# Kernel optimization log

Hardware: AMD Instinct MI355X
Metric: run time of the kernel (lower is better)

## Reference

```python
import jax, jax.numpy as jnp
import numpy as np

K = 3          # pooling factor (init k)
H_OUT = 8      # number of bilinear heads
H_DIM = 512    # hidden dim after pooling
BN_EPS = 1e-5
NEG_INF = -jnp.inf


def setup_inputs() -> dict:
    key = jax.random.key(0)
    ks = jax.random.split(key, 8)
    b, vn, qn, vd, qd = 16, 256, 256, 512, 768
    hk = H_DIM * K
    return {
        "v": jax.random.normal(ks[0], (b, vn, vd), jnp.float32),
        "q": jax.random.normal(ks[1], (b, qn, qd), jnp.float32),
        "Wv": jax.random.normal(ks[2], (hk, vd), jnp.float32) * 0.05,
        "bv": jax.random.normal(ks[3], (hk,), jnp.float32) * 0.05,
        "Wq": jax.random.normal(ks[4], (hk, qd), jnp.float32) * 0.05,
        "bq": jax.random.normal(ks[5], (hk,), jnp.float32) * 0.05,
        "h_mat": jax.random.normal(ks[6], (1, H_OUT, 1, hk), jnp.float32),
        "h_bias": jax.random.normal(ks[7], (1, H_OUT, 1, 1), jnp.float32),
        "bn_gamma": jnp.ones((H_DIM,), jnp.float32),
        "bn_beta": jnp.zeros((H_DIM,), jnp.float32),
    }


def _forward(v, q, Wv, bv, Wq, bq, h_mat, h_bias, bn_gamma, bn_beta):
    # FCNet (eval mode: dropout is identity; weight_norm folded into W)
    v_ = jax.nn.relu(jnp.einsum("bvd,kd->bvk", v, Wv) + bv)   # [b, vn, h_dim*k]
    q_ = jax.nn.relu(jnp.einsum("bqd,kd->bqk", q, Wq) + bq)   # [b, qn, h_dim*k]

    # Bilinear attention maps: [b, h_out, vn, qn]
    att = jnp.einsum("xhyk,bvk,bqk->bhvq", h_mat, v_, q_) + h_bias

    # v_mask / q_mask (all-zero token rows masked to -inf)
    v_zero = jnp.sum(jnp.abs(v), axis=2) == 0                  # [b, vn]
    q_zero = jnp.sum(jnp.abs(q), axis=2) == 0                  # [b, qn]
    att = jnp.where(v_zero[:, None, :, None], NEG_INF, att)
    att = jnp.where(q_zero[:, None, None, :], NEG_INF, att)

    # Fused per-head attention pooling, summed over heads (original Python loop)
    fused = jnp.einsum("bhvq,bqk->bhvk", att, q_)
    logits_k = jnp.einsum("bvk,bhvk->bk", v_, fused)           # [b, h_dim*k]

    # AvgPool1d(k, stride=k) * k  == sum over groups of k
    b = logits_k.shape[0]
    logits = logits_k.reshape(b, H_DIM, K).sum(axis=2)         # [b, h_dim]

    # BatchNorm1d (training-mode batch statistics, biased variance)
    mu = logits.mean(axis=0)
    var = logits.var(axis=0)
    logits = (logits - mu) * jax.lax.rsqrt(var + BN_EPS) * bn_gamma + bn_beta
    return logits, att


def reference(v, q, Wv, bv, Wq, bq, h_mat, h_bias, bn_gamma, bn_beta):
    return _forward(v, q, Wv, bv, Wq, bq, h_mat, h_bias, bn_gamma, bn_beta)
```

## Files before the change

kernel.cpp:

```cpp
#include <hip/hip_runtime.h>
#include <math.h>

#define BB    16
#define VN    256
#define QN    256
#define VD    512
#define QD    768
#define HK    1536
#define HDIM  512

typedef _Float16 half8 __attribute__((ext_vector_type(8)));
typedef _Float16 half4 __attribute__((ext_vector_type(4)));
typedef float f32x4 __attribute__((ext_vector_type(4)));

__global__ __launch_bounds__(256) void conv_mask2(
    const float* __restrict__ v, const float* __restrict__ q,
    _Float16* __restrict__ v16, _Float16* __restrict__ q16,
    float* __restrict__ vz, float* __restrict__ qz) {
    int which = blockIdx.y;
    const float* src = which ? q : v;
    _Float16* dst = which ? q16 : v16;
    float* outz = which ? qz : vz;
    int D = which ? QD : VD;
    int w = threadIdx.x >> 6, ln = threadIdx.x & 63;
    int row = blockIdx.x * 4 + w;
    const float* p = src + (size_t)row * D;
    _Float16* d = dst + (size_t)row * D;
    float s = 0.f;
    for (int c = ln * 4; c < D; c += 256) {
        float4 x = *(const float4*)(p + c);
        s += fabsf(x.x) + fabsf(x.y) + fabsf(x.z) + fabsf(x.w);
        half4 hh = {(_Float16)x.x, (_Float16)x.y, (_Float16)x.z, (_Float16)x.w};
        *(half4*)(d + c) = hh;
    }
    for (int off = 32; off > 0; off >>= 1) s += __shfl_down(s, off);
    if (ln == 0) outz[row] = (s == 0.f) ? 1.f : 0.f;
}

__global__ __launch_bounds__(256) void conv_w3(
    const float* __restrict__ Wv, _Float16* __restrict__ Wv16, int n4v,
    const float* __restrict__ Wq, _Float16* __restrict__ Wq16, int n4q,
    const float* __restrict__ hm, _Float16* __restrict__ hs16) {
    if (blockIdx.y == 2) {
        int k = blockIdx.x * 256 + threadIdx.x;
        if (k >= HK) return;
        float s = 0.f;
#pragma unroll
        for (int h = 0; h < 8; ++h) {
            float x = hm[h * HK + k];
            s += x;
            hs16[h * HK + k] = (_Float16)x;
        }
        hs16[8 * HK + k] = (_Float16)s;
        return;
    }
    const float* src = blockIdx.y ? Wq : Wv;
    _Float16* dst = blockIdx.y ? Wq16 : Wv16;
    int n4 = blockIdx.y ? n4q : n4v;
    int i = blockIdx.x * 256 + threadIdx.x;
    if (i < n4) {
        float4 x = ((const float4*)src)[i];
        half4 h = {(_Float16)x.x, (_Float16)x.y, (_Float16)x.z, (_Float16)x.w};
        ((half4*)dst)[i] = h;
    }
}

__global__ __launch_bounds__(128) void proj_lds(
    const _Float16* __restrict__ Ain, const _Float16* __restrict__ W16,
    const float* __restrict__ bias, _Float16* __restrict__ C16, int K) {
    __shared__ _Float16 As[64 * 64];
    __shared__ _Float16 Bs[64 * 64];
    int m0 = blockIdx.y * 64, n0 = blockIdx.x * 64;
    int t = threadIdx.x;
    int w = t >> 6, ln = t & 63, quad = ln >> 4, r16 = ln & 15;
    int arow = t >> 3, aseg = t & 7;
    int sg = aseg ^ (arow & 7);
    const _Float16* ApG = Ain + (size_t)(m0 + arow) * K + aseg * 8;
    const _Float16* BpG = W16 + (size_t)(n0 + arow) * K + aseg * 8;
    half8 ra[4], rb[4];
#pragma unroll
    for (int c = 0; c < 4; ++c) {
        ra[c] = *(const half8*)(ApG + (size_t)c * 16 * K);
        rb[c] = *(const half8*)(BpG + (size_t)c * 16 * K);
    }
    f32x4 acc[2][4] = {};
    for (int k0 = 0; k0 < K; k0 += 64) {
        __syncthreads();
#pragma unroll
        for (int c = 0; c < 4; ++c) {
            *(half8*)&As[(c * 16 + arow) * 64 + sg * 8] = ra[c];
            *(half8*)&Bs[(c * 16 + arow) * 64 + sg * 8] = rb[c];
        }
        __syncthreads();
        if (k0 + 64 < K) {
#pragma unroll
            for (int c = 0; c < 4; ++c) {
                ra[c] = *(const half8*)(ApG + (size_t)c * 16 * K + k0 + 64);
                rb[c] = *(const half8*)(BpG + (size_t)c * 16 * K + k0 + 64);
            }
        }
#pragma unroll
        for (int kc = 0; kc < 2; ++kc) {
            half8 af[2], bf[4];
#pragma unroll
            for (int fi = 0; fi < 2; ++fi) {
                int rl = w * 32 + fi * 16 + r16;
                af[fi] = *(const half8*)&As[rl * 64 + ((kc * 4 + quad) ^ (rl & 7)) * 8];
            }
#pragma unroll
            for (int fj = 0; fj < 4; ++fj) {
                int rl = fj * 16 + r16;
                bf[fj] = *(const half8*)&Bs[rl * 64 + ((kc * 4 + quad) ^ (rl & 7)) * 8];
            }
#pragma unroll
            for (int fi = 0; fi < 2; ++fi)
#pragma unroll
                for (int fj = 0; fj < 4; ++fj)
                    acc[fi][fj] = __builtin_amdgcn_mfma_f32_16x16x32_f16(
                        af[fi], bf[fj], acc[fi][fj], 0, 0, 0);
        }
    }
#pragma unroll
    for (int fi = 0; fi < 2; ++fi) {
#pragma unroll
        for (int r = 0; r < 4; ++r) {
            int m = m0 + w * 32 + fi * 16 + quad * 4 + r;
#pragma unroll
            for (int fj = 0; fj < 4; ++fj) {
                int n = n0 + fj * 16 + r16;
                float x = acc[fi][fj][r] + bias[n];
                C16[(size_t)m * HK + n] = (_Float16)fmaxf(x, 0.f);
            }
        }
    }
}

__global__ __launch_bounds__(256, 2) void att_db(
    const _Float16* __restrict__ v16, const _Float16* __restrict__ q16,
    const _Float16* __restrict__ hs16, const float* __restrict__ hb,
    const float* __restrict__ vz, const float* __restrict__ qz,
    float* __restrict__ att_out, _Float16* __restrict__ A16) {
    __shared__ _Float16 As[2][64 * 64];
    __shared__ _Float16 Bs[2][32 * 64];
    __shared__ _Float16 Hl[8 * HK];
    int lin = blockIdx.x;
    int swz = ((lin & 7) << 6) | (lin >> 3);
    int jb = swz & 7, ib = (swz >> 3) & 3, b = swz >> 5;
    int i0 = ib * 64, j0 = jb * 32;
    int t = threadIdx.x;
    int w = t >> 6, ln = t & 63, quad = ln >> 4, r16 = ln & 15;
    int iw = w & 1, hg = w >> 1, h0 = hg * 4;
    int arow = t >> 3, aseg = t & 7;
    int sg = (aseg ^ (arow & 7)) * 8;
    for (int u = t * 8; u < 8 * HK; u += 256 * 8)
        *(half8*)&Hl[u] = *(const half8*)(hs16 + u);
    const _Float16* ApG = v16 + (size_t)b * VN * HK + (size_t)(i0 + arow) * HK + aseg * 8;
    const _Float16* BpG = q16 + (size_t)b * QN * HK + (size_t)(j0 + arow) * HK + aseg * 8;
    half8 ra[2], rb;
    ra[0] = *(const half8*)(ApG);
    ra[1] = *(const half8*)(ApG + (size_t)32 * HK);
    rb    = *(const half8*)(BpG);
    *(half8*)&As[0][arow * 64 + sg] = ra[0];
    *(half8*)&As[0][(arow + 32) * 64 + sg] = ra[1];
    *(half8*)&Bs[0][arow * 64 + sg] = rb;
    ra[0] = *(const half8*)(ApG + 64);
    ra[1] = *(const half8*)(ApG + (size_t)32 * HK + 64);
    rb    = *(const half8*)(BpG + 64);
    f32x4 acc[4][2][2] = {};
    for (int it = 0; it < 24; ++it) {
        __syncthreads();
        int cur = it & 1;
        const _Float16* Ac = As[cur];
        const _Float16* Bc = Bs[cur];
        if (it + 1 < 24) {
            int nxt = cur ^ 1;
            *(half8*)&As[nxt][arow * 64 + sg] = ra[0];
            *(half8*)&As[nxt][(arow + 32) * 64 + sg] = ra[1];
            *(half8*)&Bs[nxt][arow * 64 + sg] = rb;
        }
        if (it + 2 < 24) {
            int kn = (it + 2) * 64;
            ra[0] = *(const half8*)(ApG + kn);
            ra[1] = *(const half8*)(ApG + (size_t)32 * HK + kn);
            rb    = *(const half8*)(BpG + kn);
        }
        int kb = it * 64;
#pragma unroll
        for (int kc = 0; kc < 2; ++kc) {
            half8 af[2], bf[2];
#pragma unroll
            for (int fi = 0; fi < 2; ++fi) {
                int rl = iw * 32 + fi * 16 + r16;
                af[fi] = *(const half8*)&Ac[rl * 64 + ((kc * 4 + quad) ^ (rl & 7)) * 8];
            }
#pragma unroll
            for (int fj = 0; fj < 2; ++fj) {
                int rl = fj * 16 + r16;
                bf[fj] = *(const half8*)&Bc[rl * 64 + ((kc * 4 + quad) ^ (rl & 7)) * 8];
            }
#pragma unroll
            for (int hh = 0; hh < 4; ++hh) {
                half8 hmv = *(const half8*)&Hl[(h0 + hh) * HK + kb + (kc * 4 + quad) * 8];
#pragma unroll
                for (int fi = 0; fi < 2; ++fi) {
                    half8 am = af[fi] * hmv;
#pragma unroll
                    for (int fj = 0; fj < 2; ++fj)
                        acc[hh][fi][fj] = __builtin_amdgcn_mfma_f32_16x16x32_f16(
                            am, bf[fj], acc[hh][fi][fj], 0, 0, 0);
                }
            }
        }
    }
    float s[2][2][4];
#pragma unroll
    for (int fi = 0; fi < 2; ++fi)
#pragma unroll
        for (int fj = 0; fj < 2; ++fj)
#pragma unroll
            for (int r = 0; r < 4; ++r) {
                float ss = 0.f;
#pragma unroll
                for (int hh = 0; hh < 4; ++hh) ss += acc[hh][fi][fj][r];
                s[fi][fj][r] = ss;
            }
    float hbv[4];
#pragma unroll
    for (int hh = 0; hh < 4; ++hh) hbv[hh] = hb[h0 + hh];
    float hbsum = 0.f;
#pragma unroll
    for (int h = 0; h < 8; ++h) hbsum += hb[h];
    float qm[2];
#pragma unroll
    for (int fj = 0; fj < 2; ++fj) qm[fj] = qz[b * QN + j0 + fj * 16 + r16];
    float* outb = att_out + (size_t)b * 8 * VN * QN;
#pragma unroll
    for (int fi = 0; fi < 2; ++fi) {
#pragma unroll
        for (int r = 0; r < 4; ++r) {
            int i = i0 + iw * 32 + fi * 16 + quad * 4 + r;
            float vm = vz[b * VN + i];
#pragma unroll
            for (int fj = 0; fj < 2; ++fj) {
                int j = j0 + fj * 16 + r16;
                bool msk = (vm != 0.f) || (qm[fj] != 0.f);
#pragma unroll
                for (int hh = 0; hh < 4; ++hh) {
                    float x = acc[hh][fi][fj][r] + hbv[hh];
                    if (msk) x = -INFINITY;
                    outb[(size_t)(h0 + hh) * VN * QN + (size_t)i * QN + j] = x;
                }
            }
        }
    }
    __syncthreads();
    float* Red = (float*)&As[0][0];
    if (hg) {
#pragma unroll
        for (int fi = 0; fi < 2; ++fi)
#pragma unroll
            for (int fj = 0; fj < 2; ++fj)
#pragma unroll
                for (int r = 0; r < 4; ++r)
                    Red[iw * 1024 + (fi * 16 + quad * 4 + r) * 32 + fj * 16 + r16] =
                        s[fi][fj][r];
    }
    __syncthreads();
    if (!hg) {
        _Float16* Ab = A16 + (size_t)b * VN * QN;
#pragma unroll
        for (int fi = 0; fi < 2; ++fi) {
#pragma unroll
            for (int r = 0; r < 4; ++r) {
                int i = i0 + iw * 32 + fi * 16 + quad * 4 + r;
                float vm = vz[b * VN + i];
#pragma unroll
                for (int fj = 0; fj < 2; ++fj) {
                    int j = j0 + fj * 16 + r16;
                    float tot = s[fi][fj][r] +
                                Red[iw * 1024 + (fi * 16 + quad * 4 + r) * 32 + fj * 16 + r16] +
                                hbsum;
                    if (vm != 0.f || qm[fj] != 0.f) tot = -INFINITY;
                    Ab[(size_t)i * QN + j] = (_Float16)tot;
                }
            }
        }
    }
}

__global__ __launch_bounds__(256) void transpose_q16(const _Float16* __restrict__ q16,
                                                     _Float16* __restrict__ q16t) {
    __shared__ _Float16 Ls[32][72];
    int b = blockIdx.z;
    int k0 = blockIdx.x * 64, j0 = blockIdx.y * 32;
    int t = threadIdx.x;
    const _Float16* src = q16 + (size_t)b * QN * HK;
    int tj = t >> 3, tk = (t & 7) * 8;
    half8 vv = *(const half8*)(src + (size_t)(j0 + tj) * HK + k0 + tk);
#pragma unroll
    for (int e = 0; e < 8; ++e) Ls[tj][tk + e] = vv[e];
    __syncthreads();
    int ok = t >> 2, oj = (t & 3) * 8;
    half8 ov;
#pragma unroll
    for (int e = 0; e < 8; ++e) ov[e] = Ls[oj + e][ok];
    *(half8*)(q16t + (size_t)b * HK * QN + (size_t)(k0 + ok) * QN + j0 + oj) = ov;
}

__global__ __launch_bounds__(256) void t_lk_mfma(
    const _Float16* __restrict__ A16, const _Float16* __restrict__ q16t,
    const _Float16* __restrict__ v16, float* __restrict__ lk) {
    __shared__ _Float16 As[256 * 32];
    __shared__ _Float16 Bs[64 * 32];
    __shared__ float red[16][64];
    int b = blockIdx.y;
    int k0 = blockIdx.x * 64;
    int t = threadIdx.x;
    int w = t >> 6, ln = t & 63, quad = ln >> 4, r16 = ln & 15;
    const _Float16* Ab = A16 + (size_t)b * VN * QN;
    const _Float16* Qt = q16t + (size_t)b * HK * QN + (size_t)k0 * QN;
    int ar = t >> 2, aseg = t & 3;
    f32x4 acc[4][4] = {};
    for (int j0 = 0; j0 < QN; j0 += 32) {
        half8 a0 = *(const half8*)(Ab + (size_t)(ar +   0) * QN + j0 + aseg * 8);
        half8 a1 = *(const half8*)(Ab + (size_t)(ar +  64) * QN + j0 + aseg * 8);
        half8 a2 = *(const half8*)(Ab + (size_t)(ar + 128) * QN + j0 + aseg * 8);
        half8 a3 = *(const half8*)(Ab + (size_t)(ar + 192) * QN + j0 + aseg * 8);
        half8 bv = *(const half8*)(Qt + (size_t)ar * QN + j0 + aseg * 8);
        __syncthreads();
        *(half8*)&As[(ar +   0) * 32 + aseg * 8] = a0;
        *(half8*)&As[(ar +  64) * 32 + aseg * 8] = a1;
        *(half8*)&As[(ar + 128) * 32 + aseg * 8] = a2;
        *(half8*)&As[(ar + 192) * 32 + aseg * 8] = a3;
        *(half8*)&Bs[ar * 32 + aseg * 8] = bv;
        __syncthreads();
        half8 af[4], bf[4];
#pragma unroll
        for (int fi = 0; fi < 4; ++fi)
            af[fi] = *(const half8*)&As[(w * 64 + fi * 16 + r16) * 32 + quad * 8];
#pragma unroll
        for (int fj = 0; fj < 4; ++fj)
            bf[fj] = *(const half8*)&Bs[(fj * 16 + r16) * 32 + quad * 8];
#pragma unroll
        for (int fi = 0; fi < 4; ++fi)
#pragma unroll
            for (int fj = 0; fj < 4; ++fj)
                acc[fi][fj] = __builtin_amdgcn_mfma_f32_16x16x32_f16(
                    af[fi], bf[fj], acc[fi][fj], 0, 0, 0);
    }
    const _Float16* Vb = v16 + (size_t)b * VN * HK;
    float part[4] = {0.f, 0.f, 0.f, 0.f};
#pragma unroll
    for (int fi = 0; fi < 4; ++fi) {
#pragma unroll
        for (int r = 0; r < 4; ++r) {
            int i = w * 64 + fi * 16 + quad * 4 + r;
#pragma unroll
            for (int fj = 0; fj < 4; ++fj) {
                float vv = (float)Vb[(size_t)i * HK + k0 + fj * 16 + r16];
                part[fj] += acc[fi][fj][r] * vv;
            }
        }
    }
#pragma unroll
    for (int fj = 0; fj < 4; ++fj)
        red[w * 4 + quad][fj * 16 + r16] = part[fj];
    __syncthreads();
    if (t < 64) {
        float s = 0.f;
#pragma unroll
        for (int g = 0; g < 16; ++g) s += red[g][t];
        lk[b * HK + k0 + t] = s;
    }
}

__global__ __launch_bounds__(256) void bn_kernel(
    const float* __restrict__ lk, const float* __restrict__ gamma,
    const float* __restrict__ beta, float* __restrict__ out) {
    int d = blockIdx.x * blockDim.x + threadIdx.x;
    if (d >= HDIM) return;
    float l[BB];
    float mu = 0.f;
#pragma unroll
    for (int b = 0; b < BB; ++b) {
        const float* p = lk + b * HK + 3 * d;
        float s = p[0] + p[1] + p[2];
        l[b] = s;
        mu += s;
    }
    mu *= (1.f / BB);
    float var = 0.f;
#pragma unroll
    for (int b = 0; b < BB; ++b) {
        float dd = l[b] - mu;
        var += dd * dd;
    }
    var *= (1.f / BB);
    float inv = rsqrtf(var + 1e-5f);
    float g = gamma[d], be = beta[d];
#pragma unroll
    for (int b = 0; b < BB; ++b)
        out[b * HDIM + d] = (l[b] - mu) * inv * g + be;
}

extern "C" void kernel_launch(void* const* d_in, const int* in_sizes, int n_in,
                              void* d_out, int out_size, void* d_ws, size_t ws_size,
                              hipStream_t stream) {
    const float* v  = (const float*)d_in[0];
    const float* q  = (const float*)d_in[1];
    const float* Wv = (const float*)d_in[2];
    const float* bv = (const float*)d_in[3];
    const float* Wq = (const float*)d_in[4];
    const float* bq = (const float*)d_in[5];
    const float* hm = (const float*)d_in[6];
    const float* hb = (const float*)d_in[7];
    const float* gamma = (const float*)d_in[8];
    const float* beta  = (const float*)d_in[9];

    float* out_logits = (float*)d_out;
    float* out_att    = out_logits + BB * HDIM;

    _Float16* h = (_Float16*)d_ws;
    _Float16* v16   = h;
    _Float16* q16   = v16 + (size_t)BB * VN * HK;
    _Float16* q16t  = q16 + (size_t)BB * QN * HK;
    _Float16* A16   = q16t + (size_t)BB * HK * QN;
    _Float16* v16in = A16 + (size_t)BB * VN * QN;
    _Float16* q16in = v16in + (size_t)BB * VN * VD;
    _Float16* Wv16  = q16in + (size_t)BB * QN * QD;
    _Float16* Wq16  = Wv16 + (size_t)HK * VD;
    _Float16* hs16  = Wq16 + (size_t)HK * QD;
    float* lk = (float*)(hs16 + 9 * HK + 8);
    float* vz = lk + BB * HK;
    float* qz = vz + BB * VN;

    conv_mask2<<<dim3(BB * VN / 4, 2), 256, 0, stream>>>(v, q, v16in, q16in, vz, qz);
    conv_w3<<<dim3((HK * QD / 4 + 255) / 256, 3), 256, 0, stream>>>(
        Wv, Wv16, HK * VD / 4, Wq, Wq16, HK * QD / 4, hm, hs16);

    proj_lds<<<dim3(HK / 64, BB * VN / 64), 128, 0, stream>>>(v16in, Wv16, bv, v16, VD);
    proj_lds<<<dim3(HK / 64, BB * QN / 64), 128, 0, stream>>>(q16in, Wq16, bq, q16, QD);

    att_db<<<dim3(512), 256, 0, stream>>>(
        v16, q16, hs16, hb, vz, qz, out_att, A16);

    transpose_q16<<<dim3(HK / 64, QN / 32, BB), 256, 0, stream>>>(q16, q16t);

    t_lk_mfma<<<dim3(HK / 64, BB), 256, 0, stream>>>(A16, q16t, v16, lk);

    bn_kernel<<<dim3((HDIM + 255) / 256), 256, 0, stream>>>(lk, gamma, beta, out_logits);
}
```

Baseline: 189.6 us.

## Enlarge projection GEMM tiles to 128x128 and merge v/q projections into one launch

Replaces the 64x64-tile, 128-thread projection kernel with a 128x128-tile, 256-thread kernel in which each wave computes a 64x64 sub-tile, which raises MFMA work per LDS load and per global load. The v and q projections now run as one launch selected by blockIdx.z, removing a launch and letting the two GEMMs share the GPU. The trade-off is more registers and LDS per block, which lowers occupancy, and fewer blocks in total (768 instead of 3072).

```diff
diff --git a/kernel.cpp b/kernel.cpp
--- a/kernel.cpp
+++ b/kernel.cpp
@@ -65,55 +65,64 @@
     }
 }
 
-__global__ __launch_bounds__(128) void proj_lds(
-    const _Float16* __restrict__ Ain, const _Float16* __restrict__ W16,
-    const float* __restrict__ bias, _Float16* __restrict__ C16, int K) {
-    __shared__ _Float16 As[64 * 64];
-    __shared__ _Float16 Bs[64 * 64];
-    int m0 = blockIdx.y * 64, n0 = blockIdx.x * 64;
+__global__ __launch_bounds__(256, 2) void proj128(
+    const _Float16* __restrict__ v16in, const _Float16* __restrict__ Wv16,
+    const float* __restrict__ bv, _Float16* __restrict__ v16,
+    const _Float16* __restrict__ q16in, const _Float16* __restrict__ Wq16,
+    const float* __restrict__ bq, _Float16* __restrict__ q16) {
+    __shared__ _Float16 As[128 * 64];
+    __shared__ _Float16 Bs[128 * 64];
+    int z = blockIdx.z;
+    const _Float16* Ain = z ? q16in : v16in;
+    const _Float16* W16 = z ? Wq16 : Wv16;
+    const float* bias = z ? bq : bv;
+    _Float16* C16 = z ? q16 : v16;
+    int K = z ? QD : VD;
+    int m0 = blockIdx.y * 128, n0 = blockIdx.x * 128;
     int t = threadIdx.x;
     int w = t >> 6, ln = t & 63, quad = ln >> 4, r16 = ln & 15;
+    int wi = w & 1, wj = w >> 1;
     int arow = t >> 3, aseg = t & 7;
-    int sg = aseg ^ (arow & 7);
+    int sg = (aseg ^ (arow & 7)) * 8;
     const _Float16* ApG = Ain + (size_t)(m0 + arow) * K + aseg * 8;
     const _Float16* BpG = W16 + (size_t)(n0 + arow) * K + aseg * 8;
     half8 ra[4], rb[4];
 #pragma unroll
     for (int c = 0; c < 4; ++c) {
-        ra[c] = *(const half8*)(ApG + (size_t)c * 16 * K);
-        rb[c] = *(const half8*)(BpG + (size_t)c * 16 * K);
-    }
-    f32x4 acc[2][4] = {};
+        ra[c] = *(const half8*)(ApG + (size_t)c * 32 * K);
+        rb[c] = *(const half8*)(BpG + (size_t)c * 32 * K);
+    }
+    f32x4 acc[4][4] = {};
     for (int k0 = 0; k0 < K; k0 += 64) {
         __syncthreads();
 #pragma unroll
         for (int c = 0; c < 4; ++c) {
-            *(half8*)&As[(c * 16 + arow) * 64 + sg * 8] = ra[c];
-            *(half8*)&Bs[(c * 16 + arow) * 64 + sg * 8] = rb[c];
+            *(half8*)&As[(c * 32 + arow) * 64 + sg] = ra[c];
+            *(half8*)&Bs[(c * 32 + arow) * 64 + sg] = rb[c];
         }
         __syncthreads();
         if (k0 + 64 < K) {
 #pragma unroll
             for (int c = 0; c < 4; ++c) {
-                ra[c] = *(const half8*)(ApG + (size_t)c * 16 * K + k0 + 64);
-                rb[c] = *(const half8*)(BpG + (size_t)c * 16 * K + k0 + 64);
+                ra[c] = *(const half8*)(ApG + (size_t)c * 32 * K + k0 + 64);
+                rb[c] = *(const half8*)(BpG + (size_t)c * 32 * K + k0 + 64);
             }
         }
 #pragma unroll
         for (int kc = 0; kc < 2; ++kc) {
-            half8 af[2], bf[4];
-#pragma unroll
-            for (int fi = 0; fi < 2; ++fi) {
-                int rl = w * 32 + fi * 16 + r16;
+            half8 af[4], bf[4];
+#pragma unroll
+            for (int fi = 0; fi < 4; ++fi) {
+                int rl = wi * 64 + fi * 16 + r16;
                 af[fi] = *(const half8*)&As[rl * 64 + ((kc * 4 + quad) ^ (rl & 7)) * 8];
             }
 #pragma unroll
             for (int fj = 0; fj < 4; ++fj) {
-                int rl = fj * 16 + r16;
+                int rl = wj * 64 + fj * 16 + r16;
                 bf[fj] = *(const half8*)&Bs[rl * 64 + ((kc * 4 + quad) ^ (rl & 7)) * 8];
             }
 #pragma unroll
-            for (int fi = 0; fi < 2; ++fi)
+            for (int fi = 0; fi < 4; ++fi)
 #pragma unroll
                 for (int fj = 0; fj < 4; ++fj)
                     acc[fi][fj] = __builtin_amdgcn_mfma_f32_16x16x32_f16(
@@ -121,13 +130,13 @@
         }
     }
 #pragma unroll
-    for (int fi = 0; fi < 2; ++fi) {
+    for (int fi = 0; fi < 4; ++fi) {
 #pragma unroll
         for (int r = 0; r < 4; ++r) {
-            int m = m0 + w * 32 + fi * 16 + quad * 4 + r;
+            int m = m0 + wi * 64 + fi * 16 + quad * 4 + r;
 #pragma unroll
             for (int fj = 0; fj < 4; ++fj) {
-                int n = n0 + fj * 16 + r16;
+                int n = n0 + wj * 64 + fj * 16 + r16;
                 float x = acc[fi][fj][r] + bias[n];
                 C16[(size_t)m * HK + n] = (_Float16)fmaxf(x, 0.f);
             }
@@ -438,8 +447,8 @@
     conv_w3<<<dim3((HK * QD / 4 + 255) / 256, 3), 256, 0, stream>>>(
         Wv, Wv16, HK * VD / 4, Wq, Wq16, HK * QD / 4, hm, hs16);
 
-    proj_lds<<<dim3(HK / 64, BB * VN / 64), 128, 0, stream>>>(v16in, Wv16, bv, v16, VD);
-    proj_lds<<<dim3(HK / 64, BB * QN / 64), 128, 0, stream>>>(q16in, Wq16, bq, q16, QD);
+    proj128<<<dim3(HK / 128, BB * VN / 128, 2), 256, 0, stream>>>(
+        v16in, Wv16, bv, v16, q16in, Wq16, bq, q16);
 
     att_db<<<dim3(512), 256, 0, stream>>>(
         v16, q16, hs16, hb, vz, qz, out_att, A16);
```

Measured after the change: 179.2 us. -5.5%, faster.
